# Kernel optimization log

Hardware: AMD Instinct MI355X
Metric: run time of the kernel (lower is better)

Reference implementation:

```python
import jax, jax.numpy as jnp
import numpy as np

N_NODES = 100000
N_EDGES = 1600000
IN_CH = 32
HID = 128
OUT_CH = 32


def _glorot(key, shape):
    fan_in, fan_out = shape[1], shape[0]
    lim = (6.0 / (fan_in + fan_out)) ** 0.5
    return jax.random.uniform(key, shape, jnp.float32, -lim, lim)


def setup_inputs() -> dict:
    key = jax.random.key(0)
    ks = jax.random.split(key, 8)
    x = jax.random.normal(ks[0], (N_NODES, IN_CH), jnp.float32)
    edge_index = jax.random.randint(ks[1], (2, N_EDGES), 0, N_NODES, jnp.int64)
    # SAGEConv params: lin_l (neighbor agg, with bias), lin_r (root, no bias)
    W1_l = _glorot(ks[2], (HID, IN_CH))
    W1_r = _glorot(ks[3], (HID, IN_CH))
    b1 = jnp.zeros((HID,), jnp.float32)
    W2_l = _glorot(ks[4], (OUT_CH, HID))
    W2_r = _glorot(ks[5], (OUT_CH, HID))
    b2 = jnp.zeros((OUT_CH,), jnp.float32)
    return {"x": x, "edge_index": edge_index,
            "W1_l": W1_l, "W1_r": W1_r, "b1": b1,
            "W2_l": W2_l, "W2_r": W2_r, "b2": b2}


def _sage_conv(x, src, dst, W_l, W_r, b):
    # mean aggregation of neighbor features j -> i over edges (src=j, dst=i)
    agg = jax.ops.segment_sum(x[src], dst, num_segments=N_NODES)  # [N, C]
    deg = jax.ops.segment_sum(jnp.ones((src.shape[0],), x.dtype), dst,
                              num_segments=N_NODES)
    agg = agg / jnp.maximum(deg, 1.0)[:, None]
    return agg @ W_l.T + x @ W_r.T + b


def reference(x, edge_index, W1_l, W1_r, b1, W2_l, W2_r, b2):
    src, dst = edge_index[0], edge_index[1]
    h = _sage_conv(x, src, dst, W1_l, W1_r, b1)
    h = jax.nn.relu(h)
    # dropout is identity in eval mode (training=False)
    out = _sage_conv(h, src, dst, W2_l, W2_r, b2)
    return out
```

## Files before the change

kernel.cpp:

```cpp
#include <hip/hip_runtime.h>
#include <hip/hip_bf16.h>

typedef __hip_bfloat16 bf16;
typedef unsigned short ush;
typedef __attribute__((ext_vector_type(8))) unsigned short ush8;
typedef __attribute__((ext_vector_type(8))) short s8v;
typedef __attribute__((ext_vector_type(4))) float f4;

#define IN_CH 32
#define HID 128
#define OUT_CH 32
#define S_CAP 32
#define OVF_CAP 80000
#define NB_MAX 2048
#define SC_CHUNK 8192

__device__ __forceinline__ float bf2f(ush u) {
    return __uint_as_float(((unsigned)u) << 16);
}
__device__ __forceinline__ ush f2bf(float f) {
    __hip_bfloat16 b = __float2bfloat16(f);
    return __builtin_bit_cast(ush, b);
}
__device__ __forceinline__ float ldf(const void* __restrict__ p, size_t idx, int isbf16) {
    return isbf16 ? bf2f(((const ush*)p)[idx]) : ((const float*)p)[idx];
}
__device__ __forceinline__ int ld_edge(const int* __restrict__ ei, size_t elem, int wide) {
    return wide ? ei[2 * elem] : ei[elem];
}

__global__ void k_detect(const unsigned short* __restrict__ xraw,
                         const int* __restrict__ ei, int* __restrict__ flags) {
    __shared__ int cnt_exp, any_nz;
    if (threadIdx.x == 0) { cnt_exp = 0; any_nz = 0; }
    __syncthreads();
    int local = 0;
    for (int k = threadIdx.x; k < 4096; k += 256) {
        int e = (xraw[k] >> 7) & 0xFF;
        if (e >= 100 && e <= 140) ++local;
    }
    atomicAdd(&cnt_exp, local);
    for (int k = threadIdx.x; k < 2048; k += 256)
        if (ei[2 * k + 1] != 0) any_nz = 1;
    __syncthreads();
    if (threadIdx.x == 0) {
        flags[0] = (cnt_exp > 3500) ? 1 : 0;
        flags[1] = any_nz ? 0 : 1;
    }
}

__global__ void k_fillp(const int* __restrict__ ei, int n_edges,
                        const int* __restrict__ flags,
                        int* __restrict__ cnt, int* __restrict__ csr,
                        int* __restrict__ ovf, int* __restrict__ ovfn) {
    int e = blockIdx.x * blockDim.x + threadIdx.x;
    if (e >= n_edges) return;
    int w = flags[1];
    int d  = ld_edge(ei, (size_t)n_edges + e, w);
    int sc = ld_edge(ei, (size_t)e, w);
    int r = atomicAdd(&cnt[d], 1);
    if (r < S_CAP) {
        csr[d * S_CAP + r] = sc;
    } else {
        int o = atomicAdd(ovfn, 1);
        if (o < OVF_CAP) { ((int2*)ovf)[o] = make_int2(d, sc); }
    }
}


__global__ __launch_bounds__(256) void k_hist(
        const int* __restrict__ ei, int n_edges,
        const int* __restrict__ flags,
        int* __restrict__ hist, int NB) {
    __shared__ int hl[NB_MAX];
    int t = threadIdx.x;
    for (int k = t; k < NB; k += 256) hl[k] = 0;
    __syncthreads();
    int w = flags[1];
    int stride = gridDim.x * 256;
    for (int e = blockIdx.x * 256 + t; e < n_edges; e += stride) {
        int d = ld_edge(ei, (size_t)n_edges + e, w);
        atomicAdd(&hl[d >> 8], 1);
    }
    __syncthreads();
    for (int k = t; k < NB; k += 256)
        if (hl[k]) atomicAdd(&hist[k], hl[k]);
}

__global__ __launch_bounds__(256) void k_scan(
        const int* __restrict__ hist,
        int* __restrict__ base, int* __restrict__ cursor, int NB) {
    __shared__ int part[256];
    int t = threadIdx.x;
    int chunk = (NB + 255) / 256;
    int lo = t * chunk, hi = min(NB, (t + 1) * chunk);
    int s = 0;
    for (int k = lo; k < hi; ++k) s += hist[k];
    part[t] = s;
    __syncthreads();
    if (t == 0) {
        int r = 0;
        for (int q = 0; q < 256; ++q) { int v = part[q]; part[q] = r; r += v; }
        base[NB] = r;
    }
    __syncthreads();
    int r = part[t];
    for (int k = lo; k < hi; ++k) {
        base[k] = r; cursor[k] = r;
        r += hist[k];
    }
}

__global__ __launch_bounds__(256) void k_scatter(
        const int* __restrict__ ei, int n_edges,
        const int* __restrict__ flags,
        int* __restrict__ cursor, int* __restrict__ pairs, int NB) {
    __shared__ int cA[NB_MAX];
    __shared__ int oA[NB_MAX];
    int t = threadIdx.x;
    int w = flags[1];
    int e0 = blockIdx.x * SC_CHUNK;
    int ecnt = min(SC_CHUNK, n_edges - e0);
    if (ecnt <= 0) return;
    for (int k = t; k < NB; k += 256) cA[k] = 0;
    __syncthreads();
    for (int k = t; k < ecnt; k += 256) {
        int d = ld_edge(ei, (size_t)n_edges + e0 + k, w);
        atomicAdd(&cA[d >> 8], 1);
    }
    __syncthreads();
    for (int b = t; b < NB; b += 256) {
        int c = cA[b];
        oA[b] = c ? atomicAdd(&cursor[b], c) : 0;
        cA[b] = 0;
    }
    __syncthreads();
    for (int k = t; k < ecnt; k += 256) {
        int d  = ld_edge(ei, (size_t)n_edges + e0 + k, w);
        int sc = ld_edge(ei, (size_t)e0 + k, w);
        int b = d >> 8;
        int r = atomicAdd(&cA[b], 1);
        pairs[oA[b] + r] = sc | ((d & 255) << 24);
    }
}

__global__ __launch_bounds__(256) void k_build(
        const int* __restrict__ pairs, const int* __restrict__ base,
        int* __restrict__ cnt, int* __restrict__ csr,
        int* __restrict__ ovf, int* __restrict__ ovfn, int n_nodes) {
    __shared__ int cntL[256];
    __shared__ int im[256 * S_CAP];
    int b = blockIdx.x;
    int t = threadIdx.x;
    cntL[t] = 0;
    __syncthreads();
    int s0 = base[b], s1 = base[b + 1];
    int node0 = b << 8;
    for (int k = s0 + t; k < s1; k += 256) {
        int v = pairs[k];
        int src = v & 0x00FFFFFF;
        int ld = ((unsigned)v) >> 24;
        int r = atomicAdd(&cntL[ld], 1);
        if (r < S_CAP) {
            im[ld * S_CAP + r] = src;
        } else {
            int o = atomicAdd(ovfn, 1);
            if (o < OVF_CAP) { ((int2*)ovf)[o] = make_int2(node0 + ld, src); }
        }
    }
    __syncthreads();
    int nvalid = min(256, n_nodes - node0);
    if (t < nvalid) cnt[node0 + t] = cntL[t];
    for (int k = t; k < nvalid * S_CAP; k += 256)
        csr[(size_t)node0 * S_CAP + k] = im[k];
}

__global__ __launch_bounds__(256, 8) void k_agg1(
        const void* __restrict__ x,
        const int* __restrict__ cnt, const int* __restrict__ csr,
        const int* __restrict__ ovf, const int* __restrict__ ovfn,
        const int* __restrict__ flags,
        float* __restrict__ aggf, ush* __restrict__ aggb, int aggf32,
        int n_nodes) {
    int fb = flags[0];
    int t = threadIdx.x;
    int wave = t >> 6, lane = t & 63;
    int g4 = lane & 60;
    int c  = lane & 3;
    int node = (blockIdx.x * 4 + wave) * 16 + (lane >> 2);
    bool valid = node < n_nodes;
    int nd = valid ? node : n_nodes - 1;
    int dg = cnt[nd];
    int lim = min(dg, S_CAP);
    int idxr[8];
    {
        int4 i0 = *(const int4*)&csr[(size_t)nd * S_CAP + c * 8];
        int4 i1 = *(const int4*)&csr[(size_t)nd * S_CAP + c * 8 + 4];
        idxr[0] = i0.x; idxr[1] = i0.y; idxr[2] = i0.z; idxr[3] = i0.w;
        idxr[4] = i1.x; idxr[5] = i1.y; idxr[6] = i1.z; idxr[7] = i1.w;
    }
    int lmax = lim;
    lmax = max(lmax, __shfl_xor(lmax, 4));
    lmax = max(lmax, __shfl_xor(lmax, 8));
    lmax = max(lmax, __shfl_xor(lmax, 16));
    lmax = max(lmax, __shfl_xor(lmax, 32));
    float acc[8] = {0, 0, 0, 0, 0, 0, 0, 0};
    if (fb) {
        const ush* xb = (const ush*)x;
        for (int kb = 0; kb < 4; ++kb) {
            if (kb * 8 >= lmax) break;
#pragma unroll
            for (int kk = 0; kk < 8; ++kk) {
                int src = __shfl(idxr[kk], g4 + kb);
                if (kb * 8 + kk < lim) {
                    ush8 v = *(const ush8*)(xb + (size_t)src * IN_CH + c * 8);
#pragma unroll
                    for (int j = 0; j < 8; ++j) acc[j] += bf2f(v[j]);
                }
            }
        }
        if (dg > S_CAP) {
            int on = min(*ovfn, OVF_CAP);
            for (int k = 0; k < on; ++k) {
                int2 pr = ((const int2*)ovf)[k];
                if (pr.x == nd && valid) {
                    ush8 v = *(const ush8*)(xb + (size_t)pr.y * IN_CH + c * 8);
#pragma unroll
                    for (int j = 0; j < 8; ++j) acc[j] += bf2f(v[j]);
                }
            }
        }
    } else {
        const float* xb = (const float*)x;
        for (int kb = 0; kb < 4; ++kb) {
            if (kb * 8 >= lmax) break;
#pragma unroll
            for (int kk = 0; kk < 8; ++kk) {
                int src = __shfl(idxr[kk], g4 + kb);
                if (kb * 8 + kk < lim) {
                    const float* rp = xb + (size_t)src * IN_CH + c * 8;
                    f4 a0 = *(const f4*)rp;
                    f4 a1 = *(const f4*)(rp + 4);
#pragma unroll
                    for (int j = 0; j < 4; ++j) { acc[j] += a0[j]; acc[4 + j] += a1[j]; }
                }
            }
        }
        if (dg > S_CAP) {
            int on = min(*ovfn, OVF_CAP);
            for (int k = 0; k < on; ++k) {
                int2 pr = ((const int2*)ovf)[k];
                if (pr.x == nd && valid) {
                    const float* rp = xb + (size_t)pr.y * IN_CH + c * 8;
                    f4 a0 = *(const f4*)rp;
                    f4 a1 = *(const f4*)(rp + 4);
#pragma unroll
                    for (int j = 0; j < 4; ++j) { acc[j] += a0[j]; acc[4 + j] += a1[j]; }
                }
            }
        }
    }
    if (valid) {
        float rd = 1.0f / (float)(dg > 1 ? dg : 1);
        if (aggf32) {
            float* op = aggf + (size_t)node * IN_CH + c * 8;
            f4 o0, o1;
#pragma unroll
            for (int j = 0; j < 4; ++j) { o0[j] = acc[j] * rd; o1[j] = acc[4 + j] * rd; }
            *(f4*)op = o0;
            *(f4*)(op + 4) = o1;
        } else {
            ush8 ov;
#pragma unroll
            for (int j = 0; j < 8; ++j) ov[j] = f2bf(acc[j] * rd);
            *(ush8*)(aggb + (size_t)node * IN_CH + c * 8) = ov;
        }
    }
}

__global__ __launch_bounds__(256, 4) void k_mm1_mfma(
        const void* __restrict__ x,
        const float* __restrict__ aggf, const ush* __restrict__ aggb, int aggf32,
        const void* __restrict__ W1l, const void* __restrict__ W1r,
        const void* __restrict__ b1,
        const int* __restrict__ flags,
        ush* __restrict__ hout, int n_nodes) {
    __shared__ ush wst[HID * 64];
    int fb = flags[0];
    int t = threadIdx.x;
    for (int idx = t; idx < HID * IN_CH; idx += 256) {
        int o = idx >> 5, c = idx & 31;
        wst[o * 64 + c]      = f2bf(ldf(W1l, idx, fb));
        wst[o * 64 + 32 + c] = f2bf(ldf(W1r, idx, fb));
    }
    __syncthreads();
    int wave = t >> 6, lane = t & 63;
    int col  = lane & 15;
    int kgrp = lane >> 4;
    s8v bfr[8][2];
    float bias[8];
#pragma unroll
    for (int tt = 0; tt < 8; ++tt) {
        int o = tt * 16 + col;
#pragma unroll
        for (int q = 0; q < 2; ++q)
            bfr[tt][q] = __builtin_bit_cast(s8v, *(const ush8*)&wst[o * 64 + q * 32 + kgrp * 8]);
        bias[tt] = ldf(b1, o, fb);
    }
    int gw = blockIdx.x * 4 + wave;
    int nw = gridDim.x * 4;
    for (int n0 = gw * 16; n0 < n_nodes; n0 += nw * 16) {
        int arow = n0 + col;
        if (arow >= n_nodes) arow = n_nodes - 1;
        s8v a0;
        if (aggf32) {
            const float* ap = aggf + (size_t)arow * IN_CH + kgrp * 8;
            f4 v0 = *(const f4*)ap;
            f4 v1 = *(const f4*)(ap + 4);
            ush8 tmp;
#pragma unroll
            for (int j = 0; j < 4; ++j) { tmp[j] = f2bf(v0[j]); tmp[4 + j] = f2bf(v1[j]); }
            a0 = __builtin_bit_cast(s8v, tmp);
        } else {
            a0 = __builtin_bit_cast(s8v, *(const ush8*)(aggb + (size_t)arow * IN_CH + kgrp * 8));
        }
        s8v a1;
        if (fb) {
            a1 = __builtin_bit_cast(s8v, *(const ush8*)((const ush*)x + (size_t)arow * IN_CH + kgrp * 8));
        } else {
            const float* rp = (const float*)x + (size_t)arow * IN_CH + kgrp * 8;
            f4 v0 = *(const f4*)rp;
            f4 v1 = *(const f4*)(rp + 4);
            ush8 tmp;
#pragma unroll
            for (int j = 0; j < 4; ++j) { tmp[j] = f2bf(v0[j]); tmp[4 + j] = f2bf(v1[j]); }
            a1 = __builtin_bit_cast(s8v, tmp);
        }
        f4 acc[8];
#pragma unroll
        for (int tt = 0; tt < 8; ++tt) {
            f4 z = {0, 0, 0, 0};
            z = __builtin_amdgcn_mfma_f32_16x16x32_bf16(a0, bfr[tt][0], z, 0, 0, 0);
            z = __builtin_amdgcn_mfma_f32_16x16x32_bf16(a1, bfr[tt][1], z, 0, 0, 0);
            acc[tt] = z;
        }
#pragma unroll
        for (int r = 0; r < 4; ++r) {
            int node = n0 + kgrp * 4 + r;
            if (node < n_nodes) {
#pragma unroll
                for (int tt = 0; tt < 8; ++tt) {
                    float v = acc[tt][r] + bias[tt];
                    hout[(size_t)node * HID + tt * 16 + col] = f2bf(v > 0.0f ? v : 0.0f);
                }
            }
        }
    }
}

__global__ __launch_bounds__(256, 4) void k_g_mfma(
        ush* __restrict__ h, ush* __restrict__ gout,
        const void* __restrict__ W2l, const void* __restrict__ W2r,
        const void* __restrict__ b2,
        const int* __restrict__ flags, int n_nodes) {
    __shared__ ush wst[2 * OUT_CH * HID];
    int fb = flags[0];
    int t = threadIdx.x;
    for (int idx = t; idx < OUT_CH * HID; idx += 256) {
        wst[idx]                  = f2bf(ldf(W2l, idx, fb));
        wst[OUT_CH * HID + idx]   = f2bf(ldf(W2r, idx, fb));
    }
    __syncthreads();
    int wave = t >> 6, lane = t & 63;
    int col  = lane & 15;
    int kgrp = lane >> 4;
    s8v bfr[4][4];
#pragma unroll
    for (int tt = 0; tt < 4; ++tt) {
        int base = (tt < 2 ? 0 : OUT_CH * HID) + ((tt & 1) * 16 + col) * HID + kgrp * 8;
#pragma unroll
        for (int q = 0; q < 4; ++q)
            bfr[tt][q] = __builtin_bit_cast(s8v, *(const ush8*)&wst[base + q * 32]);
    }
    float bias0 = ldf(b2, col, fb);
    float bias1 = ldf(b2, 16 + col, fb);
    int gw = blockIdx.x * 4 + wave;
    int nw = gridDim.x * 4;
    for (int n0 = gw * 16; n0 < n_nodes; n0 += nw * 16) {
        int arow = n0 + col;
        if (arow >= n_nodes) arow = n_nodes - 1;
        const ush* hp = h + (size_t)arow * HID + kgrp * 8;
        s8v a0 = __builtin_bit_cast(s8v, *(const ush8*)(hp));
        s8v a1 = __builtin_bit_cast(s8v, *(const ush8*)(hp + 32));
        s8v a2 = __builtin_bit_cast(s8v, *(const ush8*)(hp + 64));
        s8v a3 = __builtin_bit_cast(s8v, *(const ush8*)(hp + 96));
        f4 acc0 = {0, 0, 0, 0}, acc1 = {0, 0, 0, 0}, acc2 = {0, 0, 0, 0}, acc3 = {0, 0, 0, 0};
        acc0 = __builtin_amdgcn_mfma_f32_16x16x32_bf16(a0, bfr[0][0], acc0, 0, 0, 0);
        acc0 = __builtin_amdgcn_mfma_f32_16x16x32_bf16(a1, bfr[0][1], acc0, 0, 0, 0);
        acc0 = __builtin_amdgcn_mfma_f32_16x16x32_bf16(a2, bfr[0][2], acc0, 0, 0, 0);
        acc0 = __builtin_amdgcn_mfma_f32_16x16x32_bf16(a3, bfr[0][3], acc0, 0, 0, 0);
        acc1 = __builtin_amdgcn_mfma_f32_16x16x32_bf16(a0, bfr[1][0], acc1, 0, 0, 0);
        acc1 = __builtin_amdgcn_mfma_f32_16x16x32_bf16(a1, bfr[1][1], acc1, 0, 0, 0);
        acc1 = __builtin_amdgcn_mfma_f32_16x16x32_bf16(a2, bfr[1][2], acc1, 0, 0, 0);
        acc1 = __builtin_amdgcn_mfma_f32_16x16x32_bf16(a3, bfr[1][3], acc1, 0, 0, 0);
        acc2 = __builtin_amdgcn_mfma_f32_16x16x32_bf16(a0, bfr[2][0], acc2, 0, 0, 0);
        acc2 = __builtin_amdgcn_mfma_f32_16x16x32_bf16(a1, bfr[2][1], acc2, 0, 0, 0);
        acc2 = __builtin_amdgcn_mfma_f32_16x16x32_bf16(a2, bfr[2][2], acc2, 0, 0, 0);
        acc2 = __builtin_amdgcn_mfma_f32_16x16x32_bf16(a3, bfr[2][3], acc2, 0, 0, 0);
        acc3 = __builtin_amdgcn_mfma_f32_16x16x32_bf16(a0, bfr[3][0], acc3, 0, 0, 0);
        acc3 = __builtin_amdgcn_mfma_f32_16x16x32_bf16(a1, bfr[3][1], acc3, 0, 0, 0);
        acc3 = __builtin_amdgcn_mfma_f32_16x16x32_bf16(a2, bfr[3][2], acc3, 0, 0, 0);
        acc3 = __builtin_amdgcn_mfma_f32_16x16x32_bf16(a3, bfr[3][3], acc3, 0, 0, 0);
#pragma unroll
        for (int r = 0; r < 4; ++r) {
            int node = n0 + kgrp * 4 + r;
            if (node < n_nodes) {
                gout[(size_t)node * OUT_CH + col]      = f2bf(acc0[r]);
                gout[(size_t)node * OUT_CH + 16 + col] = f2bf(acc1[r]);
                h[(size_t)node * HID + 32 + col]       = f2bf(acc2[r] + bias0);
                h[(size_t)node * HID + 48 + col]       = f2bf(acc3[r] + bias1);
            }
        }
    }
}

__global__ __launch_bounds__(256, 8) void k_l2g(
        const ush* __restrict__ gbuf, const ush* __restrict__ hs,
        const int* __restrict__ cnt, const int* __restrict__ csr,
        const int* __restrict__ ovf, const int* __restrict__ ovfn,
        const int* __restrict__ flags,
        void* __restrict__ out, int n_nodes) {
    int fb = flags[0];
    int t = threadIdx.x;
    int wave = t >> 6, lane = t & 63;
    int g4 = lane & 60;
    int c  = lane & 3;
    int node = (blockIdx.x * 4 + wave) * 16 + (lane >> 2);
    bool valid = node < n_nodes;
    int nd = valid ? node : n_nodes - 1;
    int dg = cnt[nd];
    int lim = min(dg, S_CAP);
    int idxr[8];
    {
        int4 i0 = *(const int4*)&csr[(size_t)nd * S_CAP + c * 8];
        int4 i1 = *(const int4*)&csr[(size_t)nd * S_CAP + c * 8 + 4];
        idxr[0] = i0.x; idxr[1] = i0.y; idxr[2] = i0.z; idxr[3] = i0.w;
        idxr[4] = i1.x; idxr[5] = i1.y; idxr[6] = i1.z; idxr[7] = i1.w;
    }
    int lmax = lim;
    lmax = max(lmax, __shfl_xor(lmax, 4));
    lmax = max(lmax, __shfl_xor(lmax, 8));
    lmax = max(lmax, __shfl_xor(lmax, 16));
    lmax = max(lmax, __shfl_xor(lmax, 32));
    float acc[8] = {0, 0, 0, 0, 0, 0, 0, 0};
    for (int kb = 0; kb < 4; ++kb) {
        if (kb * 8 >= lmax) break;
#pragma unroll
        for (int kk = 0; kk < 8; ++kk) {
            int src = __shfl(idxr[kk], g4 + kb);
            if (kb * 8 + kk < lim) {
                ush8 v = *(const ush8*)(gbuf + (size_t)src * OUT_CH + c * 8);
#pragma unroll
                for (int j = 0; j < 8; ++j) acc[j] += bf2f(v[j]);
            }
        }
    }
    if (dg > S_CAP) {
        int on = min(*ovfn, OVF_CAP);
        for (int k = 0; k < on; ++k) {
            int2 pr = ((const int2*)ovf)[k];
            if (pr.x == nd && valid) {
                ush8 v = *(const ush8*)(gbuf + (size_t)pr.y * OUT_CH + c * 8);
#pragma unroll
                for (int j = 0; j < 8; ++j) acc[j] += bf2f(v[j]);
            }
        }
    }
    if (valid) {
        float rd = 1.0f / (float)(dg > 1 ? dg : 1);
        ush8 selfv = *(const ush8*)(hs + (size_t)node * HID + 32 + c * 8);
        if (fb) {
            ush8 ov;
#pragma unroll
            for (int j = 0; j < 8; ++j)
                ov[j] = f2bf(acc[j] * rd + bf2f(selfv[j]));
            *(ush8*)((ush*)out + (size_t)node * OUT_CH + c * 8) = ov;
        } else {
            float* op = (float*)out + (size_t)node * OUT_CH + c * 8;
            f4 a0, a1;
#pragma unroll
            for (int j = 0; j < 4; ++j) {
                a0[j] = acc[j] * rd + bf2f(selfv[j]);
                a1[j] = acc[4 + j] * rd + bf2f(selfv[4 + j]);
            }
            *(f4*)op = a0;
            *(f4*)(op + 4) = a1;
        }
    }
}

extern "C" void kernel_launch(void* const* d_in, const int* in_sizes, int n_in,
                              void* d_out, int out_size, void* d_ws, size_t ws_size,
                              hipStream_t stream) {
    const void* x   = d_in[0];
    const int*  ei  = (const int*)d_in[1];
    const void* W1l = d_in[2];
    const void* W1r = d_in[3];
    const void* b1  = d_in[4];
    const void* W2l = d_in[5];
    const void* W2r = d_in[6];
    const void* b2  = d_in[7];

    int n_nodes = in_sizes[0] / IN_CH;
    int n_edges = in_sizes[1] / 2;

    char* ws = (char*)d_ws;
    size_t o_cnt = 256;
    size_t o_csr = (o_cnt + (size_t)n_nodes * 4 + 127) & ~(size_t)127;
    size_t o_ovf = (o_csr + ((size_t)n_nodes * S_CAP + 64) * 4 + 127) & ~(size_t)127;
    size_t o_hist = o_ovf + (size_t)OVF_CAP * 8;
    size_t o_h   = (o_hist + (size_t)(3 * (NB_MAX + 2)) * 4 + 255) & ~(size_t)255;
    size_t o_gb  = (o_h + (size_t)n_nodes * HID * 2 + 255) & ~(size_t)255;
    size_t o_ag  = (o_gb + (size_t)n_nodes * OUT_CH * 2 + 255) & ~(size_t)255;
    size_t need_f32 = o_ag + (size_t)n_nodes * IN_CH * 4;

    int* flags = (int*)ws;
    int* ovfn  = (int*)(ws + 128);
    int* cnt   = (int*)(ws + o_cnt);
    int* csr   = (int*)(ws + o_csr);
    int* ovf   = (int*)(ws + o_ovf);
    int* hist  = (int*)(ws + o_hist);
    int* base  = hist + NB_MAX;
    int* curs  = base + NB_MAX + 1;
    ush* h     = (ush*)(ws + o_h);
    int* pairs = (int*)(ws + o_h);
    ush* gbuf  = (ush*)(ws + o_gb);

    int aggf32 = (ws_size >= need_f32) ? 1 : 0;
    float* aggf = (float*)(ws + o_ag);
    ush*   aggb = gbuf;

    int NB = (n_nodes + 255) >> 8;
    int use_bucket = (NB <= NB_MAX) && (n_nodes < (1 << 24)) &&
                     ((size_t)n_edges * 4 <= (size_t)n_nodes * HID * 2) && (n_edges > 0);

    hipMemsetAsync(ws, 0, 256, stream);

    k_detect<<<1, 256, 0, stream>>>((const unsigned short*)x, ei, flags);

    if (use_bucket) {
        hipMemsetAsync(hist, 0, (size_t)NB * 4, stream);
        int nchunks = (n_edges + SC_CHUNK - 1) / SC_CHUNK;
        k_hist<<<256, 256, 0, stream>>>(ei, n_edges, flags, hist, NB);
        k_scan<<<1, 256, 0, stream>>>(hist, base, curs, NB);
        k_scatter<<<nchunks, 256, 0, stream>>>(ei, n_edges, flags, curs, pairs, NB);
        k_build<<<NB, 256, 0, stream>>>(pairs, base, cnt, csr, ovf, ovfn, n_nodes);
    } else {
        hipMemsetAsync(cnt, 0, (size_t)n_nodes * 4, stream);
        k_fillp<<<(n_edges + 255) / 256, 256, 0, stream>>>(ei, n_edges, flags, cnt, csr, ovf, ovfn);
    }

    int nblk_g = (n_nodes + 63) / 64;
    k_agg1<<<nblk_g, 256, 0, stream>>>(x, cnt, csr, ovf, ovfn, flags, aggf, aggb, aggf32, n_nodes);
    k_mm1_mfma<<<1024, 256, 0, stream>>>(x, aggf, aggb, aggf32, W1l, W1r, b1, flags, h, n_nodes);
    k_g_mfma<<<1024, 256, 0, stream>>>(h, gbuf, W2l, W2r, b2, flags, n_nodes);
    k_l2g<<<nblk_g, 256, 0, stream>>>(gbuf, h, cnt, csr, ovf, ovfn, flags, d_out, n_nodes);
}
```

Baseline: 233.8 us.

## Use 128-node buckets, bf16 aggregate buffer, and dense self-term buffer

```diff
diff --git a/kernel.cpp b/kernel.cpp
--- a/kernel.cpp
+++ b/kernel.cpp
@@ -13,7 +13,7 @@
 #define S_CAP 32
 #define OVF_CAP 80000
 #define NB_MAX 2048
-#define SC_CHUNK 8192
+#define SC_CHUNK 4096
 
 __device__ __forceinline__ float bf2f(ush u) {
     return __uint_as_float(((unsigned)u) << 16);
@@ -80,7 +80,7 @@
     int stride = gridDim.x * 256;
     for (int e = blockIdx.x * 256 + t; e < n_edges; e += stride) {
         int d = ld_edge(ei, (size_t)n_edges + e, w);
-        atomicAdd(&hl[d >> 8], 1);
+        atomicAdd(&hl[d >> 7], 1);
     }
     __syncthreads();
     for (int k = t; k < NB; k += 256)
@@ -126,7 +126,7 @@
     __syncthreads();
     for (int k = t; k < ecnt; k += 256) {
         int d = ld_edge(ei, (size_t)n_edges + e0 + k, w);
-        atomicAdd(&cA[d >> 8], 1);
+        atomicAdd(&cA[d >> 7], 1);
     }
     __syncthreads();
     for (int b = t; b < NB; b += 256) {
@@ -138,9 +138,9 @@
     for (int k = t; k < ecnt; k += 256) {
         int d  = ld_edge(ei, (size_t)n_edges + e0 + k, w);
         int sc = ld_edge(ei, (size_t)e0 + k, w);
-        int b = d >> 8;
+        int b = d >> 7;
         int r = atomicAdd(&cA[b], 1);
-        pairs[oA[b] + r] = sc | ((d & 255) << 24);
+        pairs[oA[b] + r] = sc | ((d & 127) << 25);
     }
 }
 
@@ -148,18 +148,18 @@
         const int* __restrict__ pairs, const int* __restrict__ base,
         int* __restrict__ cnt, int* __restrict__ csr,
         int* __restrict__ ovf, int* __restrict__ ovfn, int n_nodes) {
-    __shared__ int cntL[256];
-    __shared__ int im[256 * S_CAP];
+    __shared__ int cntL[128];
+    __shared__ int im[128 * S_CAP];
     int b = blockIdx.x;
     int t = threadIdx.x;
-    cntL[t] = 0;
+    if (t < 128) cntL[t] = 0;
     __syncthreads();
     int s0 = base[b], s1 = base[b + 1];
-    int node0 = b << 8;
+    int node0 = b << 7;
     for (int k = s0 + t; k < s1; k += 256) {
         int v = pairs[k];
-        int src = v & 0x00FFFFFF;
-        int ld = ((unsigned)v) >> 24;
+        int src = v & 0x01FFFFFF;
+        int ld = ((unsigned)v) >> 25;
         int r = atomicAdd(&cntL[ld], 1);
         if (r < S_CAP) {
             im[ld * S_CAP + r] = src;
@@ -169,7 +169,7 @@
         }
     }
     __syncthreads();
-    int nvalid = min(256, n_nodes - node0);
+    int nvalid = min(128, n_nodes - node0);
     if (t < nvalid) cnt[node0 + t] = cntL[t];
     for (int k = t; k < nvalid * S_CAP; k += 256)
         csr[(size_t)node0 * S_CAP + k] = im[k];
@@ -180,8 +180,7 @@
         const int* __restrict__ cnt, const int* __restrict__ csr,
         const int* __restrict__ ovf, const int* __restrict__ ovfn,
         const int* __restrict__ flags,
-        float* __restrict__ aggf, ush* __restrict__ aggb, int aggf32,
-        int n_nodes) {
+        ush* __restrict__ aggb, int n_nodes) {
     int fb = flags[0];
     int t = threadIdx.x;
     int wave = t >> 6, lane = t & 63;
@@ -262,25 +261,15 @@
     }
     if (valid) {
         float rd = 1.0f / (float)(dg > 1 ? dg : 1);
-        if (aggf32) {
-            float* op = aggf + (size_t)node * IN_CH + c * 8;
-            f4 o0, o1;
-#pragma unroll
-            for (int j = 0; j < 4; ++j) { o0[j] = acc[j] * rd; o1[j] = acc[4 + j] * rd; }
-            *(f4*)op = o0;
-            *(f4*)(op + 4) = o1;
-        } else {
-            ush8 ov;
-#pragma unroll
-            for (int j = 0; j < 8; ++j) ov[j] = f2bf(acc[j] * rd);
-            *(ush8*)(aggb + (size_t)node * IN_CH + c * 8) = ov;
-        }
+        ush8 ov;
+#pragma unroll
+        for (int j = 0; j < 8; ++j) ov[j] = f2bf(acc[j] * rd);
+        *(ush8*)(aggb + (size_t)node * IN_CH + c * 8) = ov;
     }
 }
 
 __global__ __launch_bounds__(256, 4) void k_mm1_mfma(
-        const void* __restrict__ x,
-        const float* __restrict__ aggf, const ush* __restrict__ aggb, int aggf32,
+        const void* __restrict__ x, const ush* __restrict__ aggb,
         const void* __restrict__ W1l, const void* __restrict__ W1r,
         const void* __restrict__ b1,
         const int* __restrict__ flags,
@@ -312,18 +301,7 @@
     for (int n0 = gw * 16; n0 < n_nodes; n0 += nw * 16) {
         int arow = n0 + col;
         if (arow >= n_nodes) arow = n_nodes - 1;
-        s8v a0;
-        if (aggf32) {
-            const float* ap = aggf + (size_t)arow * IN_CH + kgrp * 8;
-            f4 v0 = *(const f4*)ap;
-            f4 v1 = *(const f4*)(ap + 4);
-            ush8 tmp;
-#pragma unroll
-            for (int j = 0; j < 4; ++j) { tmp[j] = f2bf(v0[j]); tmp[4 + j] = f2bf(v1[j]); }
-            a0 = __builtin_bit_cast(s8v, tmp);
-        } else {
-            a0 = __builtin_bit_cast(s8v, *(const ush8*)(aggb + (size_t)arow * IN_CH + kgrp * 8));
-        }
+        s8v a0 = __builtin_bit_cast(s8v, *(const ush8*)(aggb + (size_t)arow * IN_CH + kgrp * 8));
         s8v a1;
         if (fb) {
             a1 = __builtin_bit_cast(s8v, *(const ush8*)((const ush*)x + (size_t)arow * IN_CH + kgrp * 8));
@@ -360,6 +338,7 @@
 
 __global__ __launch_bounds__(256, 4) void k_g_mfma(
         ush* __restrict__ h, ush* __restrict__ gout,
+        ush* __restrict__ sb, int sdense,
         const void* __restrict__ W2l, const void* __restrict__ W2r,
         const void* __restrict__ b2,
         const int* __restrict__ flags, int n_nodes) {
@@ -417,8 +396,13 @@
             if (node < n_nodes) {
                 gout[(size_t)node * OUT_CH + col]      = f2bf(acc0[r]);
                 gout[(size_t)node * OUT_CH + 16 + col] = f2bf(acc1[r]);
-                h[(size_t)node * HID + 32 + col]       = f2bf(acc2[r] + bias0);
-                h[(size_t)node * HID + 48 + col]       = f2bf(acc3[r] + bias1);
+                if (sdense) {
+                    sb[(size_t)node * OUT_CH + col]      = f2bf(acc2[r] + bias0);
+                    sb[(size_t)node * OUT_CH + 16 + col] = f2bf(acc3[r] + bias1);
+                } else {
+                    h[(size_t)node * HID + 32 + col]     = f2bf(acc2[r] + bias0);
+                    h[(size_t)node * HID + 48 + col]     = f2bf(acc3[r] + bias1);
+                }
             }
         }
     }
@@ -426,6 +410,7 @@
 
 __global__ __launch_bounds__(256, 8) void k_l2g(
         const ush* __restrict__ gbuf, const ush* __restrict__ hs,
+        const ush* __restrict__ sb, int sdense,
         const int* __restrict__ cnt, const int* __restrict__ csr,
         const int* __restrict__ ovf, const int* __restrict__ ovfn,
         const int* __restrict__ flags,
@@ -478,7 +463,9 @@
     }
     if (valid) {
         float rd = 1.0f / (float)(dg > 1 ? dg : 1);
-        ush8 selfv = *(const ush8*)(hs + (size_t)node * HID + 32 + c * 8);
+        ush8 selfv = sdense
+            ? *(const ush8*)(sb + (size_t)node * OUT_CH + c * 8)
+            : *(const ush8*)(hs + (size_t)node * HID + 32 + c * 8);
         if (fb) {
             ush8 ov;
 #pragma unroll
@@ -522,7 +509,9 @@
     size_t o_h   = (o_hist + (size_t)(3 * (NB_MAX + 2)) * 4 + 255) & ~(size_t)255;
     size_t o_gb  = (o_h + (size_t)n_nodes * HID * 2 + 255) & ~(size_t)255;
     size_t o_ag  = (o_gb + (size_t)n_nodes * OUT_CH * 2 + 255) & ~(size_t)255;
-    size_t need_f32 = o_ag + (size_t)n_nodes * IN_CH * 4;
+    size_t o_sb  = (o_ag + (size_t)n_nodes * IN_CH * 2 + 255) & ~(size_t)255;
+    size_t need_agg = o_ag + (size_t)n_nodes * IN_CH * 2;
+    size_t need_sd  = o_sb + (size_t)n_nodes * OUT_CH * 2;
 
     int* flags = (int*)ws;
     int* ovfn  = (int*)(ws + 128);
@@ -536,12 +525,12 @@
     int* pairs = (int*)(ws + o_h);
     ush* gbuf  = (ush*)(ws + o_gb);
 
-    int aggf32 = (ws_size >= need_f32) ? 1 : 0;
-    float* aggf = (float*)(ws + o_ag);
-    ush*   aggb = gbuf;
-
-    int NB = (n_nodes + 255) >> 8;
-    int use_bucket = (NB <= NB_MAX) && (n_nodes < (1 << 24)) &&
+    ush* aggb  = (ws_size >= need_agg) ? (ush*)(ws + o_ag) : gbuf;
+    int  sdense = (ws_size >= need_sd) ? 1 : 0;
+    ush* sbuf  = (ush*)(ws + o_sb);
+
+    int NB = (n_nodes + 127) >> 7;
+    int use_bucket = (NB <= NB_MAX) && (n_nodes < (1 << 25)) &&
                      ((size_t)n_edges * 4 <= (size_t)n_nodes * HID * 2) && (n_edges > 0);
 
     hipMemsetAsync(ws, 0, 256, stream);
@@ -551,7 +540,7 @@
     if (use_bucket) {
         hipMemsetAsync(hist, 0, (size_t)NB * 4, stream);
         int nchunks = (n_edges + SC_CHUNK - 1) / SC_CHUNK;
-        k_hist<<<256, 256, 0, stream>>>(ei, n_edges, flags, hist, NB);
+        k_hist<<<512, 256, 0, stream>>>(ei, n_edges, flags, hist, NB);
         k_scan<<<1, 256, 0, stream>>>(hist, base, curs, NB);
         k_scatter<<<nchunks, 256, 0, stream>>>(ei, n_edges, flags, curs, pairs, NB);
         k_build<<<NB, 256, 0, stream>>>(pairs, base, cnt, csr, ovf, ovfn, n_nodes);
@@ -561,8 +550,8 @@
     }
 
     int nblk_g = (n_nodes + 63) / 64;
-    k_agg1<<<nblk_g, 256, 0, stream>>>(x, cnt, csr, ovf, ovfn, flags, aggf, aggb, aggf32, n_nodes);
-    k_mm1_mfma<<<1024, 256, 0, stream>>>(x, aggf, aggb, aggf32, W1l, W1r, b1, flags, h, n_nodes);
-    k_g_mfma<<<1024, 256, 0, stream>>>(h, gbuf, W2l, W2r, b2, flags, n_nodes);
-    k_l2g<<<nblk_g, 256, 0, stream>>>(gbuf, h, cnt, csr, ovf, ovfn, flags, d_out, n_nodes);
-}
+    k_agg1<<<nblk_g, 256, 0, stream>>>(x, cnt, csr, ovf, ovfn, flags, aggb, n_nodes);
+    k_mm1_mfma<<<1024, 256, 0, stream>>>(x, aggb, W1l, W1r, b1, flags, h, n_nodes);
+    k_g_mfma<<<1024, 256, 0, stream>>>(h, gbuf, sbuf, sdense, W2l, W2r, b2, flags, n_nodes);
+    k_l2g<<<nblk_g, 256, 0, stream>>>(gbuf, h, sbuf, sdense, cnt, csr, ovf, ovfn, flags, d_out, n_nodes);
+}
```

Result: no change. 237.7 us (+1.7%).
